# Kernel tuning notes

Measured on AMD Instinct MI355X. Metric: run time of the kernel, lower is better.

## Reference

```python
import jax, jax.numpy as jnp
import numpy as np

B, T, D, U = 64, 512, 32, 512
SIG_DIM = D + D * D  # depth-2 signature: level-1 (D) + level-2 (D*D)


def setup_inputs() -> dict:
    key = jax.random.key(0)
    k0, k1, k2, k3 = jax.random.split(key, 4)
    return {
        "x": jax.random.normal(k0, (B, T, D), jnp.float32),
        "input_kernel": jax.random.normal(k1, (D, 3 * U), jnp.float32) * 0.05,
        "recurrent_kernel": jax.random.normal(k2, (U, 3 * U), jnp.float32) * 0.05,
        "forget_kernel": jax.random.normal(k3, (SIG_DIM, U), jnp.float32) * 0.05,
        "bias": jnp.zeros((4 * U,), jnp.float32),
    }


def _signature_stream(x):
    """Depth-2 streamed path signature via Chen's identity.
    x: (B, T, D) -> (B, T-1, D + D*D); entry t is signature of path x[:, :t+2].
    For a linear segment with increment dx: level1 += dx,
    level2 += S1 (x) dx + dx (x) dx / 2.
    """
    dx = x[:, 1:] - x[:, :-1]  # (B, T-1, D)
    b, _, d = dx.shape

    def step(carry, dxt):
        S1, S2 = carry
        S2n = S2 + S1[:, :, None] * dxt[:, None, :] + 0.5 * dxt[:, :, None] * dxt[:, None, :]
        S1n = S1 + dxt
        out = jnp.concatenate([S1n, S2n.reshape(b, d * d)], axis=-1)
        return (S1n, S2n), out

    init = (jnp.zeros((b, d), dx.dtype), jnp.zeros((b, d, d), dx.dtype))
    _, stream = jax.lax.scan(step, init, jnp.swapaxes(dx, 0, 1))  # (T-1, B, S)
    return jnp.swapaxes(stream, 0, 1)


def reference(x, input_kernel, recurrent_kernel, forget_kernel, bias):
    units = recurrent_kernel.shape[0]
    b_i, b_f, b_c, b_o = jnp.split(bias, 4)

    sigs = _signature_stream(x)  # (B, T-1, S)
    t_idx = jnp.arange(1, sigs.shape[1] + 1, dtype=sigs.dtype)[None, :, None]
    norm_sigs = jnp.concatenate([jnp.zeros_like(sigs[:, :1]), sigs / t_idx], axis=1)  # (B, T, S)

    # Precompute time-parallel parts: input projection and forget gate.
    x_proj = jnp.einsum('bti,ij->btj', x, input_kernel)                        # (B, T, 3U)
    f_all = jax.nn.sigmoid(jnp.einsum('bts,su->btu', norm_sigs, forget_kernel) + b_f)  # (B, T, U)

    def step(carry, inp):
        h, c = carry
        x_t, f_t = inp
        gates = h @ recurrent_kernel + x_t
        i_t, c_hat, o_t = jnp.split(gates, 3, axis=-1)
        i_t = jax.nn.sigmoid(i_t + b_i)
        c_hat = jnp.tanh(c_hat + b_c)
        o_t = jax.nn.sigmoid(o_t + b_o)
        c_new = f_t * c + i_t * c_hat
        h_new = o_t * jnp.tanh(c_new)
        return (h_new, c_new), None

    init = (jnp.zeros((x.shape[0], units), x.dtype),
            jnp.zeros((x.shape[0], units), x.dtype))
    (h_n, c_n), _ = jax.lax.scan(step, init,
                                 (jnp.swapaxes(x_proj, 0, 1), jnp.swapaxes(f_all, 0, 1)))
    return h_n  # (B, U): return_sequences=False, return_state=False
```

## Files before the change

kernel.cpp:

```cpp
#include <hip/hip_runtime.h>

#define B_ 64
#define T_ 512
#define D_ 32
#define U_ 512
#define SIGD 1056

typedef _Float16 half8 __attribute__((ext_vector_type(8)));
typedef float f32x4 __attribute__((ext_vector_type(4)));
typedef unsigned int u32x4 __attribute__((ext_vector_type(4)));
typedef unsigned short ushort_t;
typedef unsigned int uint_t;
typedef unsigned long long ull_t;

#define SIG_OFF   0ull
#define F_OFF     69206016ull
#define FLG_OFF   102760448ull
#define A_OFF     136314880ull
#define DX_OFF    140509184ull
#define X16_OFF   144703488ull
#define R16_OFF   146800640ull
#define WF16_OFF  148471808ull
#define HB_OFF    149553152ull

__global__ __launch_bounds__(256) void k_prep(const float* __restrict__ x,
                                              _Float16* x16, float* a_buf, float* dx_buf,
                                              uint_t* hb, uint_t* flg) {
  int b = blockIdx.x;
  int tid = threadIdx.x;
  if (b >= 64) {
    for (int gi = (b - 64) * 256 + tid; gi < 163840; gi += 1024) {
      if (gi < 32768) hb[gi] = 0u;
      else flg[gi - 32768] = 0u;
    }
    return;
  }
  if (tid >= 32) return;
  int i = tid;
  float xprev = x[(b * T_) * D_ + i];
  x16[(0 * B_ + b) * D_ + i] = (_Float16)xprev;
  a_buf[(b * T_) * D_ + i] = 0.f;
  dx_buf[(b * T_) * D_ + i] = 0.f;
  float S1 = 0.f;
  for (int t = 1; t < T_; ++t) {
    float xv = x[(b * T_ + t) * D_ + i];
    float dx = xv - xprev;
    float a = S1 + 0.5f * dx;
    S1 += dx;
    a_buf[(b * T_ + t) * D_ + i] = a;
    dx_buf[(b * T_ + t) * D_ + i] = dx;
    x16[(t * B_ + b) * D_ + i] = (_Float16)xv;
    xprev = xv;
  }
}

__global__ __launch_bounds__(256) void k_weights(const float* __restrict__ rk,
                                                 const float* __restrict__ ik,
                                                 const float* __restrict__ fk,
                                                 _Float16* R16t, _Float16* Wf16) {
  int e = (blockIdx.x * 256 + threadIdx.x) * 4;
  if (e < 835584) {
    const float* src = (e < 786432) ? (rk + e) : (ik + (e - 786432));
#pragma unroll
    for (int j = 0; j < 4; ++j) R16t[e + j] = (_Float16)src[j];
  } else {
    int e2 = e - 835584;
#pragma unroll
    for (int j = 0; j < 4; ++j) Wf16[e2 + j] = (_Float16)fk[e2 + j];
  }
}

__global__ __launch_bounds__(1024) void k_sig(const float* __restrict__ a_buf,
                                              const float* __restrict__ dx_buf,
                                              _Float16* __restrict__ sig) {
  int b = blockIdx.x;
  int tid = threadIdx.x;
  int i = tid >> 5, j = tid & 31;
  __shared__ float a_ch[32][32];
  __shared__ float dx_ch[32][32];
  float S2 = 0.f;
  for (int t0 = 0; t0 < T_; t0 += 32) {
    a_ch[i][j]  = a_buf[(b * T_ + t0 + i) * D_ + j];
    dx_ch[i][j] = dx_buf[(b * T_ + t0 + i) * D_ + j];
    __syncthreads();
#pragma unroll 4
    for (int tt = 0; tt < 32; ++tt) {
      int t = t0 + tt;
      S2 += a_ch[tt][i] * dx_ch[tt][j];
      float inv = (t == 0) ? 0.f : (1.0f / (float)t);
      int row = b * T_ + t;
      sig[row * SIGD + 32 + i * 32 + j] = (_Float16)(S2 * inv);
      if (i == 0) {
        float s1 = a_ch[tt][j] + 0.5f * dx_ch[tt][j];
        sig[row * SIGD + j] = (_Float16)(s1 * inv);
      }
    }
    __syncthreads();
  }
}

__global__ __launch_bounds__(256) void k_fgemm(const _Float16* __restrict__ sig,
                                               const _Float16* __restrict__ Wf16,
                                               const float* __restrict__ bias,
                                               _Float16* __restrict__ f_buf) {
  const int tid = threadIdx.x;
  const int m0 = blockIdx.x * 64;
  const int n0 = blockIdx.y * 128;
  __shared__ __align__(16) ushort_t As[64 * 40];
  __shared__ __align__(16) ushort_t Bs[128 * 40];
  const uint_t* sig32 = (const uint_t*)sig;
  const uint_t* w32 = (const uint_t*)Wf16;
  f32x4 acc[8];
#pragma unroll
  for (int nt = 0; nt < 8; ++nt) acc[nt] = f32x4{0.f, 0.f, 0.f, 0.f};
  const int lane = tid & 63, w = tid >> 6;
  const int cl = lane & 15, q8 = (lane >> 4) * 8;
  for (int kt = 0; kt < 33; ++kt) {
#pragma unroll
    for (int it = 0; it < 4; ++it) {
      int idx = tid + (it << 8);
      int row = idx >> 4, kp = idx & 15;
      uint_t v = sig32[(m0 + row) * 528 + kt * 16 + kp];
      *(uint_t*)&As[row * 40 + kp * 2] = v;
    }
#pragma unroll
    for (int it = 0; it < 8; ++it) {
      int idx = tid + (it << 8);
      int kr = idx >> 6, np = idx & 63;
      uint_t v = w32[(kt * 32 + kr) * 256 + (n0 >> 1) + np];
      Bs[(np * 2) * 40 + kr] = (ushort_t)(v & 0xffffu);
      Bs[(np * 2 + 1) * 40 + kr] = (ushort_t)(v >> 16);
    }
    __syncthreads();
    half8 a = *(const half8*)&As[(w * 16 + cl) * 40 + q8];
#pragma unroll
    for (int nt = 0; nt < 8; ++nt) {
      half8 bfr = *(const half8*)&Bs[(nt * 16 + cl) * 40 + q8];
      acc[nt] = __builtin_amdgcn_mfma_f32_16x16x32_f16(a, bfr, acc[nt], 0, 0, 0);
    }
    __syncthreads();
  }
#pragma unroll
  for (int nt = 0; nt < 8; ++nt) {
    int col = n0 + nt * 16 + cl;
    float bf = bias[512 + col];
#pragma unroll
    for (int r = 0; r < 4; ++r) {
      int m = m0 + w * 16 + ((lane >> 4) << 2) + r;
      int t = m & 511, b = m >> 9;
      float z = acc[nt][r] + bf;
      float fv = 1.f / (1.f + __expf(-z));
      f_buf[(t * 512 + col) * 64 + b] = (_Float16)fv;
    }
  }
}

__global__ __launch_bounds__(256, 1) void k_scan(const _Float16* __restrict__ R16t,
                                                 const float* __restrict__ bias,
                                                 const _Float16* __restrict__ f16,
                                                 const _Float16* __restrict__ x16,
                                                 uint_t* hb, uint_t* flg,
                                                 float* __restrict__ out) {
  const int tid = threadIdx.x;
  const int bid = blockIdx.x;
  const int G = bid & 7;
  const int mj = bid >> 3;
  const int lane = tid & 63, w = tid >> 6;
  const int cl = lane & 15, quad = lane >> 4, q8 = quad * 8;
  const int widx = (mj << 2) | w;
  const int u0 = widx * 16;
  const int u = u0 + cl;
  const int b0 = G * 8;

  const int srcl = ((lane >> 5) & 1) * 16 + (lane & 7) * 2;
  const int rsel = (lane >> 3) & 3;

  __shared__ __align__(16) char hlds[2][8 * 1040];

  half8 bfr[3][17];
#pragma unroll
  for (int g3 = 0; g3 < 3; ++g3)
#pragma unroll
    for (int kk = 0; kk < 17; ++kk)
#pragma unroll
      for (int jj = 0; jj < 8; ++jj)
        bfr[g3][kk][jj] = R16t[(kk * 32 + q8 + jj) * 1536 + g3 * 512 + u];

  const float bi = bias[u];
  const float bc = bias[1024 + u];
  const float bo = bias[1536 + u];
  float c_st[4] = {0.f, 0.f, 0.f, 0.f};

#pragma unroll 1
  for (int t = 0; t < T_; ++t) {
    float fpre[4];
    {
      union { ull_t q; _Float16 h[4]; } fu;
      fu.q = *(const ull_t*)(f16 + ((t * 512 + u) * 64 + b0 + (quad & 1) * 4));
#pragma unroll
      for (int r = 0; r < 4; ++r) fpre[r] = (float)fu.h[r];
    }
    half8 xa = *(const half8*)(x16 + ((t * 64 + b0 + (cl & 7)) * 32 + q8));

    f32x4 ai = f32x4{0.f, 0.f, 0.f, 0.f};
    f32x4 ac = f32x4{0.f, 0.f, 0.f, 0.f};
    f32x4 ao = f32x4{0.f, 0.f, 0.f, 0.f};
    ai = __builtin_amdgcn_mfma_f32_16x16x32_f16(xa, bfr[0][16], ai, 0, 0, 0);
    ac = __builtin_amdgcn_mfma_f32_16x16x32_f16(xa, bfr[1][16], ac, 0, 0, 0);
    ao = __builtin_amdgcn_mfma_f32_16x16x32_f16(xa, bfr[2][16], ao, 0, 0, 0);

    uint_t* hb_w32 = hb + ((t & 1) ? 0 : 16384);

    if (t > 0) {
      const uint_t target = 32u * (uint_t)t;
      const uint_t* cp = flg + (G << 6);
      int spins = 0;
      for (;;) {
        uint_t v = __hip_atomic_load(cp, __ATOMIC_RELAXED, __HIP_MEMORY_SCOPE_AGENT);
        if (v >= target) break;
        if (++spins > 16) __builtin_amdgcn_s_sleep(1);
        if (spins > (1 << 18)) break;
      }
      {
        const char* src = (const char*)hb + ((t & 1) ? 65536 : 0)
                        + (unsigned)b0 * 1024 + (unsigned)tid * 16;
        const char* src2 = src + 4096;
        u32x4 s0, s1;
        asm volatile("global_load_dwordx4 %0, %2, off sc0 sc1\n\t"
                     "global_load_dwordx4 %1, %3, off sc0 sc1"
                     : "=&v"(s0), "=&v"(s1) : "v"(src), "v"(src2) : "memory");
        asm volatile("s_waitcnt vmcnt(0)" ::: "memory");
        __builtin_amdgcn_sched_barrier(0);
        int r0 = tid >> 6, cb = (tid & 63) * 16;
        char* dst = &hlds[t & 1][0];
        *(u32x4*)(dst + r0 * 1040 + cb) = s0;
        *(u32x4*)(dst + (r0 + 4) * 1040 + cb) = s1;
      }
      __syncthreads();
      const char* lbase = &hlds[t & 1][(cl & 7) * 1040 + quad * 16];
#pragma unroll
      for (int kk = 0; kk < 16; ++kk) {
        half8 af = *(const half8*)(lbase + kk * 64);
        ai = __builtin_amdgcn_mfma_f32_16x16x32_f16(af, bfr[0][kk], ai, 0, 0, 0);
        ac = __builtin_amdgcn_mfma_f32_16x16x32_f16(af, bfr[1][kk], ac, 0, 0, 0);
        ao = __builtin_amdgcn_mfma_f32_16x16x32_f16(af, bfr[2][kk], ao, 0, 0, 0);
      }
    }

    ushort_t hu0, hu1, hu2, hu3;
#define EPI_R(r, HU) { \
      float iv = 1.f / (1.f + __expf(-(ai[r] + bi))); \
      float cv = 1.f - 2.f / (__expf(2.f * (ac[r] + bc)) + 1.f); \
      float ov = 1.f / (1.f + __expf(-(ao[r] + bo))); \
      float c = fpre[r] * c_st[r] + iv * cv; \
      c_st[r] = c; \
      float h = ov * (1.f - 2.f / (__expf(2.f * c) + 1.f)); \
      HU = __builtin_bit_cast(ushort_t, (_Float16)h); \
      if (t == T_ - 1) { \
        int brow = (quad << 2) + r; \
        if (brow < 8) out[((b0 + brow) << 9) + u] = h; \
      } \
    }
    EPI_R(0, hu0) EPI_R(1, hu1) EPI_R(2, hu2) EPI_R(3, hu3)
#undef EPI_R

    if (t < T_ - 1) {
      uint_t d0 = ((uint_t)(ushort_t)__shfl((int)hu0, srcl) & 0xffffu) |
                  ((uint_t)(ushort_t)__shfl((int)hu0, srcl + 1) << 16);
      uint_t d1 = ((uint_t)(ushort_t)__shfl((int)hu1, srcl) & 0xffffu) |
                  ((uint_t)(ushort_t)__shfl((int)hu1, srcl + 1) << 16);
      uint_t d2 = ((uint_t)(ushort_t)__shfl((int)hu2, srcl) & 0xffffu) |
                  ((uint_t)(ushort_t)__shfl((int)hu2, srcl + 1) << 16);
      uint_t d3 = ((uint_t)(ushort_t)__shfl((int)hu3, srcl) & 0xffffu) |
                  ((uint_t)(ushort_t)__shfl((int)hu3, srcl + 1) << 16);
      uint_t dd = (rsel == 0) ? d0 : (rsel == 1) ? d1 : (rsel == 2) ? d2 : d3;
      int row = b0 + (lane >> 3);
      uint_t* p = hb_w32 + row * 256 + (u0 >> 1) + (lane & 7);
      __hip_atomic_store(p, dd, __ATOMIC_RELAXED, __HIP_MEMORY_SCOPE_AGENT);
      asm volatile("s_waitcnt vmcnt(0)" ::: "memory");
      if (lane == 0)
        __hip_atomic_fetch_add(flg + (G << 6), 1u, __ATOMIC_RELAXED,
                               __HIP_MEMORY_SCOPE_AGENT);
    }
  }
}

extern "C" void kernel_launch(void* const* d_in, const int* in_sizes, int n_in,
                              void* d_out, int out_size, void* d_ws, size_t ws_size,
                              hipStream_t stream) {
  const float* x = (const float*)d_in[0];
  const float* ik = (const float*)d_in[1];
  const float* rk = (const float*)d_in[2];
  const float* fk = (const float*)d_in[3];
  const float* bias = (const float*)d_in[4];
  char* ws = (char*)d_ws;
  _Float16* sig = (_Float16*)(ws + SIG_OFF);
  _Float16* f_buf = (_Float16*)(ws + F_OFF);
  uint_t* flg = (uint_t*)(ws + FLG_OFF);
  float* a_buf = (float*)(ws + A_OFF);
  float* dx_buf = (float*)(ws + DX_OFF);
  _Float16* x16 = (_Float16*)(ws + X16_OFF);
  _Float16* R16t = (_Float16*)(ws + R16_OFF);
  _Float16* Wf16 = (_Float16*)(ws + WF16_OFF);
  uint_t* hb = (uint_t*)(ws + HB_OFF);
  float* out = (float*)d_out;

  hipLaunchKernelGGL(k_prep, dim3(68), dim3(256), 0, stream, x, x16, a_buf, dx_buf, hb, flg);
  hipLaunchKernelGGL(k_weights, dim3(1344), dim3(256), 0, stream, rk, ik, fk, R16t, Wf16);
  hipLaunchKernelGGL(k_sig, dim3(64), dim3(1024), 0, stream, a_buf, dx_buf, sig);
  hipLaunchKernelGGL(k_fgemm, dim3(512, 4), dim3(256), 0, stream, sig, Wf16, bias, f_buf);
  hipLaunchKernelGGL(k_scan, dim3(64), dim3(256), 0, stream, R16t, bias, f_buf,
                     x16, hb, flg, out);
}
```

Measured before the change: 1.875 ms.

## Replace counter-flag barrier with per-word step tags packed alongside hidden state

Each hidden-state word is now stored as a 64-bit pair of fp16 data plus the step index, so readers poll the data itself instead of waiting on a shared atomic counter. This drops the vmcnt wait and the atomic fetch_add on the producer side. Consumer loads are issued at the top of the step, before the input MFMAs, and only the stale chunks are reloaded. The cost is twice the traffic for the hidden-state buffer, plus a dependence on 64-bit stores being seen atomically.

```diff
diff --git a/kernel.cpp b/kernel.cpp
--- a/kernel.cpp
+++ b/kernel.cpp
@@ -15,24 +15,20 @@
 
 #define SIG_OFF   0ull
 #define F_OFF     69206016ull
-#define FLG_OFF   102760448ull
+#define HB2_OFF   102760448ull
 #define A_OFF     136314880ull
 #define DX_OFF    140509184ull
 #define X16_OFF   144703488ull
 #define R16_OFF   146800640ull
 #define WF16_OFF  148471808ull
-#define HB_OFF    149553152ull
 
 __global__ __launch_bounds__(256) void k_prep(const float* __restrict__ x,
                                               _Float16* x16, float* a_buf, float* dx_buf,
-                                              uint_t* hb, uint_t* flg) {
+                                              uint_t* hb2) {
   int b = blockIdx.x;
   int tid = threadIdx.x;
   if (b >= 64) {
-    for (int gi = (b - 64) * 256 + tid; gi < 163840; gi += 1024) {
-      if (gi < 32768) hb[gi] = 0u;
-      else flg[gi - 32768] = 0u;
-    }
+    for (int gi = (b - 64) * 256 + tid; gi < 65536; gi += 1024) hb2[gi] = 0u;
     return;
   }
   if (tid >= 32) return;
@@ -159,15 +155,14 @@
                                                  const float* __restrict__ bias,
                                                  const _Float16* __restrict__ f16,
                                                  const _Float16* __restrict__ x16,
-                                                 uint_t* hb, uint_t* flg,
+                                                 uint_t* hb2,
                                                  float* __restrict__ out) {
   const int tid = threadIdx.x;
   const int bid = blockIdx.x;
   const int G = bid & 7;
-  const int mj = bid >> 3;
   const int lane = tid & 63, w = tid >> 6;
   const int cl = lane & 15, quad = lane >> 4, q8 = quad * 8;
-  const int widx = (mj << 2) | w;
+  const int widx = ((bid >> 3) << 2) | w;
   const int u0 = widx * 16;
   const int u = u0 + cl;
   const int b0 = G * 8;
@@ -193,6 +188,14 @@
 
 #pragma unroll 1
   for (int t = 0; t < T_; ++t) {
+    u32x4 q0, q1, q2, q3;
+    const char* src = (const char*)hb2 + ((t & 1) ? 131072 : 0)
+                    + (unsigned)b0 * 2048 + (unsigned)tid * 64;
+#define TLD(Q, OFF) \
+    asm volatile("global_load_dwordx4 %0, %1, off offset:" #OFF " sc0 sc1" \
+                 : "=&v"(Q) : "v"(src) : "memory")
+    if (t > 0) { TLD(q0, 0); TLD(q1, 16); TLD(q2, 32); TLD(q3, 48); }
+
     float fpre[4];
     {
       union { ull_t q; _Float16 h[4]; } fu;
@@ -209,33 +212,29 @@
     ac = __builtin_amdgcn_mfma_f32_16x16x32_f16(xa, bfr[1][16], ac, 0, 0, 0);
     ao = __builtin_amdgcn_mfma_f32_16x16x32_f16(xa, bfr[2][16], ao, 0, 0, 0);
 
-    uint_t* hb_w32 = hb + ((t & 1) ? 0 : 16384);
-
     if (t > 0) {
-      const uint_t target = 32u * (uint_t)t;
-      const uint_t* cp = flg + (G << 6);
-      int spins = 0;
+      const uint_t texp = (uint_t)t;
+      int rounds = 0;
       for (;;) {
-        uint_t v = __hip_atomic_load(cp, __ATOMIC_RELAXED, __HIP_MEMORY_SCOPE_AGENT);
-        if (v >= target) break;
-        if (++spins > 16) __builtin_amdgcn_s_sleep(1);
-        if (spins > (1 << 18)) break;
-      }
-      {
-        const char* src = (const char*)hb + ((t & 1) ? 65536 : 0)
-                        + (unsigned)b0 * 1024 + (unsigned)tid * 16;
-        const char* src2 = src + 4096;
-        u32x4 s0, s1;
-        asm volatile("global_load_dwordx4 %0, %2, off sc0 sc1\n\t"
-                     "global_load_dwordx4 %1, %3, off sc0 sc1"
-                     : "=&v"(s0), "=&v"(s1) : "v"(src), "v"(src2) : "memory");
         asm volatile("s_waitcnt vmcnt(0)" ::: "memory");
         __builtin_amdgcn_sched_barrier(0);
-        int r0 = tid >> 6, cb = (tid & 63) * 16;
-        char* dst = &hlds[t & 1][0];
-        *(u32x4*)(dst + r0 * 1040 + cb) = s0;
-        *(u32x4*)(dst + (r0 + 4) * 1040 + cb) = s1;
+        uint_t s0 = (q0[1] ^ texp) | (q0[3] ^ texp);
+        uint_t s1 = (q1[1] ^ texp) | (q1[3] ^ texp);
+        uint_t s2 = (q2[1] ^ texp) | (q2[3] ^ texp);
+        uint_t s3 = (q3[1] ^ texp) | (q3[3] ^ texp);
+        if ((s0 | s1 | s2 | s3) == 0u) break;
+        if (++rounds > 4096) break;
+        if (rounds > 8) __builtin_amdgcn_s_sleep(1);
+        if (s0) TLD(q0, 0);
+        if (s1) TLD(q1, 16);
+        if (s2) TLD(q2, 32);
+        if (s3) TLD(q3, 48);
       }
+      u32x4 w0{q0[0], q0[2], q1[0], q1[2]};
+      u32x4 w1{q2[0], q2[2], q3[0], q3[2]};
+      char* dst = &hlds[t & 1][(tid >> 5) * 1040 + (tid & 31) * 32];
+      *(u32x4*)dst = w0;
+      *(u32x4*)(dst + 16) = w1;
       __syncthreads();
       const char* lbase = &hlds[t & 1][(cl & 7) * 1040 + quad * 16];
 #pragma unroll
@@ -246,6 +245,7 @@
         ao = __builtin_amdgcn_mfma_f32_16x16x32_f16(af, bfr[2][kk], ao, 0, 0, 0);
       }
     }
+#undef TLD
 
     ushort_t hu0, hu1, hu2, hu3;
 #define EPI_R(r, HU) { \
@@ -275,12 +275,10 @@
                   ((uint_t)(ushort_t)__shfl((int)hu3, srcl + 1) << 16);
       uint_t dd = (rsel == 0) ? d0 : (rsel == 1) ? d1 : (rsel == 2) ? d2 : d3;
       int row = b0 + (lane >> 3);
-      uint_t* p = hb_w32 + row * 256 + (u0 >> 1) + (lane & 7);
-      __hip_atomic_store(p, dd, __ATOMIC_RELAXED, __HIP_MEMORY_SCOPE_AGENT);
-      asm volatile("s_waitcnt vmcnt(0)" ::: "memory");
-      if (lane == 0)
-        __hip_atomic_fetch_add(flg + (G << 6), 1u, __ATOMIC_RELAXED,
-                               __HIP_MEMORY_SCOPE_AGENT);
+      ull_t pk = (ull_t)dd | ((ull_t)(uint_t)(t + 1) << 32);
+      ull_t* p = (ull_t*)((char*)hb2 + ((t & 1) ? 0 : 131072)
+                          + (unsigned)row * 2048 + ((u0 >> 1) + (lane & 7)) * 8);
+      __hip_atomic_store(p, pk, __ATOMIC_RELAXED, __HIP_MEMORY_SCOPE_AGENT);
     }
   }
 }
@@ -296,19 +294,18 @@
   char* ws = (char*)d_ws;
   _Float16* sig = (_Float16*)(ws + SIG_OFF);
   _Float16* f_buf = (_Float16*)(ws + F_OFF);
-  uint_t* flg = (uint_t*)(ws + FLG_OFF);
+  uint_t* hb2 = (uint_t*)(ws + HB2_OFF);
   float* a_buf = (float*)(ws + A_OFF);
   float* dx_buf = (float*)(ws + DX_OFF);
   _Float16* x16 = (_Float16*)(ws + X16_OFF);
   _Float16* R16t = (_Float16*)(ws + R16_OFF);
   _Float16* Wf16 = (_Float16*)(ws + WF16_OFF);
-  uint_t* hb = (uint_t*)(ws + HB_OFF);
   float* out = (float*)d_out;
 
-  hipLaunchKernelGGL(k_prep, dim3(68), dim3(256), 0, stream, x, x16, a_buf, dx_buf, hb, flg);
+  hipLaunchKernelGGL(k_prep, dim3(68), dim3(256), 0, stream, x, x16, a_buf, dx_buf, hb2);
   hipLaunchKernelGGL(k_weights, dim3(1344), dim3(256), 0, stream, rk, ik, fk, R16t, Wf16);
   hipLaunchKernelGGL(k_sig, dim3(64), dim3(1024), 0, stream, a_buf, dx_buf, sig);
   hipLaunchKernelGGL(k_fgemm, dim3(512, 4), dim3(256), 0, stream, sig, Wf16, bias, f_buf);
   hipLaunchKernelGGL(k_scan, dim3(64), dim3(256), 0, stream, R16t, bias, f_buf,
-                     x16, hb, flg, out);
-}
+                     x16, hb2, out);
+}
```

Result: slower. 2.105 ms (+12.2%).
